# Kernel tuning notes

Measured on AMD Instinct MI355X. Metric: run time of the kernel, lower is better.

## Reference

```python
import jax, jax.numpy as jnp
import numpy as np

B = 1024      # Monte-Carlo samples (batch)
NX, NY = 8, 8 # lattice size
I = 3         # local Hilbert dim (hole, down, up)
H = 256       # hidden_dim
N_TARGET = 48 # target particle number
SZ = 0        # target magnetization sector


def setup_inputs() -> dict:
    key = jax.random.key(0)
    ks = jax.random.split(key, 8)
    f = jnp.float32
    samples = jax.random.randint(ks[0], (B, NX, NY), 0, 3)
    s_in = 1.0 / np.sqrt(2 * H)
    W1 = jax.random.normal(ks[1], (2 * I, 2 * H, H), f) * s_in
    W2 = jax.random.normal(ks[2], (2 * I, 2 * H, H), f) * s_in
    Wmerge = jax.random.normal(ks[3], (2 * H, H), f) * s_in
    b1 = jnp.full((H,), 0.01, f)
    b2 = jnp.full((H,), 0.01, f)
    s_l = 1.0 / np.sqrt(H)
    Wl1 = jax.random.normal(ks[4], (H, I), f) * s_l
    bl1 = jnp.zeros((I,), f)
    Wl2 = jax.random.normal(ks[5], (H, I), f) * s_l
    bl2 = jnp.zeros((I,), f)
    return {"samples": samples, "W1": W1, "b1": b1, "W2": W2, "b2": b2,
            "Wmerge": Wmerge, "Wl1": Wl1, "bl1": bl1, "Wl2": Wl2, "bl2": bl2}


def _gru_cell(sx, sy, hx, hy, W1, b1, W2, b2, Wmerge):
    # sx,sy: [B,I] one-hot neighbor inputs; hx,hy: [B,H] neighbor hiddens
    st = jnp.concatenate([hx, hy], axis=1)   # [B, 2H]
    inp = jnp.concatenate([sx, sy], axis=1)  # [B, 2I]
    # torch: einsum('ijk,lj->ikl', W, st) then einsum('li,ikl->lk', inp, .)
    pre1 = jnp.einsum('li,ijk,lj->lk', inp, W1, st)
    h_tilde = jnp.tanh(pre1 + b1)
    pre2 = jnp.einsum('li,ijk,lj->lk', inp, W2, st)
    u = jax.nn.sigmoid(pre2 + b2)
    return u * h_tilde + (1.0 - u) * (st @ Wmerge)


def _forward(samples, W1, b1, W2, b2, Wmerge, Wl1, bl1, Wl2, bl2):
    f = W1.dtype
    oh = jax.nn.one_hot(samples, I, dtype=f)  # [B,NX,NY,I]
    z_h = jnp.zeros((B, H), f)
    z_s = jnp.zeros((B, I), f)
    hid = {}
    bl_up = (N_TARGET + 2 * SZ) // 2
    bl_dn = (N_TARGET - 2 * SZ) // 2
    bl_hole = NX * NY - N_TARGET
    n_up = jnp.zeros((B,), f)
    n_dn = jnp.zeros((B,), f)
    log_a = jnp.zeros((B,), f)
    log_p = jnp.zeros((B,), f)
    k = 0  # number of already-sampled sites (static per step)
    for ny in range(NY):
        # snake (zig-zag) ordering over the 2D lattice
        xs = range(NX) if ny % 2 == 0 else range(NX - 1, -1, -1)
        dx = -1 if ny % 2 == 0 else 1
        for nx in xs:
            nxn = nx + dx
            sx = oh[:, nxn, ny] if 0 <= nxn < NX else z_s
            hx = hid.get((nxn, ny), z_h)
            sy = oh[:, nx, ny - 1] if ny > 0 else z_s
            hy = hid.get((nx, ny - 1), z_h)
            h = _gru_cell(sx, sy, hx, hy, W1, b1, W2, b2, Wmerge)
            hid[(nx, ny)] = h
            probs = jax.nn.softmax(h @ Wl1 + bl1, axis=1)          # [B,I]
            phase = jnp.pi * jax.nn.soft_sign(h @ Wl2 + bl2)       # [B,I]
            # enforce particle-number / magnetization sectors (heaviside masks)
            m_up = (bl_up - n_up > 0).astype(f)
            m_dn = (bl_dn - n_dn > 0).astype(f)
            m_hole = (bl_hole - (k - n_up - n_dn) > 0).astype(f)
            mask = jnp.stack([m_hole, m_dn, m_up], axis=1)         # [B,I]
            amp = probs * mask
            amp = amp / jnp.maximum(amp.sum(axis=1, keepdims=True), 1e-30)
            s = samples[:, nx, ny]
            sel = jax.nn.one_hot(s, I, dtype=f)
            log_a = log_a + jnp.log(jnp.clip((amp * sel).sum(axis=1), 1e-12))
            log_p = log_p + (phase * sel).sum(axis=1)
            n_up = n_up + (s == 2).astype(f)
            n_dn = n_dn + (s == 1).astype(f)
            k += 1
    return 0.5 * log_a, log_p


def reference(samples, W1, b1, W2, b2, Wmerge, Wl1, bl1, Wl2, bl2):
    return _forward(samples, W1, b1, W2, b2, Wmerge, Wl1, bl1, Wl2, bl2)
```

## Files before the change

kernel.cpp:

```cpp
#include <hip/hip_runtime.h>
#include <math.h>

#define Bsz 1024
#define Hd  256
#define MAXTILE 40
#define PERM_PER_CELL (MAXTILE*32)
#define WCSTRIDE (512*768)
#define GHALF (Bsz*768)
#define NPART 4

__global__ __launch_bounds__(256)
void build_wc(const float* __restrict__ W1, const float* __restrict__ W2,
              const float* __restrict__ Wm, float* __restrict__ Wc)
{
    size_t idx = (size_t)blockIdx.x * 256 + threadIdx.x;
    int col = (int)(idx % 768);
    size_t rem = idx / 768;
    int j = (int)(rem % 512);
    int c = (int)(rem / 512);
    int a = c >> 2, b = c & 3;
    float v;
    if (col < 256) {
        v = ((a < 3) ? W1[(size_t)a * 512 * 256 + j * 256 + col] : 0.f)
          + ((b < 3) ? W1[(size_t)(3 + b) * 512 * 256 + j * 256 + col] : 0.f);
    } else if (col < 512) {
        int cc = col - 256;
        v = ((a < 3) ? W2[(size_t)a * 512 * 256 + j * 256 + cc] : 0.f)
          + ((b < 3) ? W2[(size_t)(3 + b) * 512 * 256 + j * 256 + cc] : 0.f);
    } else {
        v = Wm[(size_t)j * 256 + (col - 512)];
    }
    Wc[idx] = v;
}

__global__ __launch_bounds__(256)
void bucketize(const int* __restrict__ samples, int* __restrict__ perm,
               int* __restrict__ tiletab)
{
    const int cell = blockIdx.x;
    const int t = threadIdx.x;
    const int ny = cell >> 3, ixs = cell & 7;
    const int nx  = (ny & 1) ? (7 - ixs) : ixs;
    const int dx  = (ny & 1) ? 1 : -1;
    const int nxn = nx + dx;
    const bool hasX = (nxn >= 0) && (nxn < 8);
    const bool hasY = (ny > 0);
    const int sx_off = nxn * 8 + ny;
    const int sy_off = nx * 8 + ny - 1;

    __shared__ int hist[16], cursor[16];
    int* pcell = perm + (size_t)cell * PERM_PER_CELL;
    for (int i = t; i < PERM_PER_CELL; i += 256) pcell[i] = -1;
    if (t < 16) hist[t] = 0;
    __syncthreads();

    int myc[4];
#pragma unroll
    for (int q = 0; q < 4; q++) {
        int l = t * 4 + q;
        int a = hasX ? samples[l * 64 + sx_off] : 3;
        int b = hasY ? samples[l * 64 + sy_off] : 3;
        myc[q] = a * 4 + b;
        atomicAdd(&hist[myc[q]], 1);
    }
    __syncthreads();

    if (t == 0) {
        int tile = 0, row = 0;
        for (int c = 0; c < 16; c++) {
            cursor[c] = row;
            int nt = (hist[c] + 31) >> 5;
            for (int k = 0; k < nt; k++) tiletab[cell * MAXTILE + tile + k] = c;
            tile += nt;
            row  += nt * 32;
        }
        for (; tile < MAXTILE; tile++) tiletab[cell * MAXTILE + tile] = -1;
    }
    __syncthreads();

#pragma unroll
    for (int q = 0; q < 4; q++) {
        int l = t * 4 + q;
        int pos = atomicAdd(&cursor[myc[q]], 1);
        pcell[pos] = l;
    }
}

#define BM 32
#define BN 64
#define BKt 32

__global__ __launch_bounds__(128)
void gemm_cell(const float* __restrict__ hx, const float* __restrict__ hy,
               const float* __restrict__ Wc, const int* __restrict__ perm,
               const int* __restrict__ tiletab, float* __restrict__ Gp,
               int cell, int kbeg, int kend)
{
    const int combo = tiletab[cell * MAXTILE + blockIdx.y];
    if (combo < 0) return;
    const int chunk = blockIdx.z;
    const int kbase = chunk << 7;
    const int hoff  = (chunk < 2) ? 0 : 256;
    int lo = (kbeg > kbase) ? kbeg : kbase;
    int hi = kbase + 128; if (kend < hi) hi = kend;
    const float* hsrc = (chunk < 2) ? hx : hy;
    const int k0 = blockIdx.x * BN;
    const float* Wsrc = Wc + (size_t)combo * WCSTRIDE;
    const int* pr = perm + (size_t)cell * PERM_PER_CELL + blockIdx.y * BM;
    float* Gout = Gp + (size_t)chunk * GHALF;

    const int t  = threadIdx.x;
    const int ar = t >> 2;
    const int aj = (t & 3) * 8;
    const int bj = t >> 4;
    const int bc = (t & 15) * 4;
    const int ty = t >> 4;
    const int tx = t & 15;

    __shared__ float As[BKt][BM];
    __shared__ float Bs[BKt][BN];
    __shared__ int rowidx[BM];
    if (t < BM) rowidx[t] = pr[t];
    const int myrow = pr[ar];

    float acc[4][4];
#pragma unroll
    for (int i = 0; i < 4; i++)
#pragma unroll
        for (int j = 0; j < 4; j++) acc[i][j] = 0.0f;

    for (int kk = lo; kk < hi; kk += BKt) {
        float4 a0 = make_float4(0.f, 0.f, 0.f, 0.f), a1 = a0;
        if (myrow >= 0) {
            const float* ap = hsrc + (size_t)myrow * Hd + (kk - hoff) + aj;
            a0 = *reinterpret_cast<const float4*>(ap);
            a1 = *reinterpret_cast<const float4*>(ap + 4);
        }
        const float* bp = Wsrc + (size_t)(kk + bj) * 768 + k0 + bc;
        float4 b0 = *reinterpret_cast<const float4*>(bp);
        float4 b1 = *reinterpret_cast<const float4*>(bp +  8 * 768);
        float4 b2 = *reinterpret_cast<const float4*>(bp + 16 * 768);
        float4 b3 = *reinterpret_cast<const float4*>(bp + 24 * 768);

        __syncthreads();
        As[aj + 0][ar] = a0.x; As[aj + 1][ar] = a0.y;
        As[aj + 2][ar] = a0.z; As[aj + 3][ar] = a0.w;
        As[aj + 4][ar] = a1.x; As[aj + 5][ar] = a1.y;
        As[aj + 6][ar] = a1.z; As[aj + 7][ar] = a1.w;
        *reinterpret_cast<float4*>(&Bs[bj     ][bc]) = b0;
        *reinterpret_cast<float4*>(&Bs[bj +  8][bc]) = b1;
        *reinterpret_cast<float4*>(&Bs[bj + 16][bc]) = b2;
        *reinterpret_cast<float4*>(&Bs[bj + 24][bc]) = b3;
        __syncthreads();

#pragma unroll
        for (int j = 0; j < BKt; j++) {
            float4 a = *reinterpret_cast<const float4*>(&As[j][ty * 4]);
            float4 b = *reinterpret_cast<const float4*>(&Bs[j][tx * 4]);
            float aa[4] = {a.x, a.y, a.z, a.w};
            float bb[4] = {b.x, b.y, b.z, b.w};
#pragma unroll
            for (int i = 0; i < 4; i++)
#pragma unroll
                for (int jj = 0; jj < 4; jj++)
                    acc[i][jj] = fmaf(aa[i], bb[jj], acc[i][jj]);
        }
    }
    __syncthreads();

#pragma unroll
    for (int i = 0; i < 4; i++) {
        int r = rowidx[ty * 4 + i];
        if (r >= 0) {
            float* gp = Gout + (size_t)r * 768 + k0 + tx * 4;
            float4 o = {acc[i][0], acc[i][1], acc[i][2], acc[i][3]};
            *reinterpret_cast<float4*>(gp) = o;
        }
    }
}

__global__ __launch_bounds__(256)
void combine_logprob(const float* __restrict__ Gp, const int* __restrict__ samples,
                     const float* __restrict__ b1, const float* __restrict__ b2,
                     const float* __restrict__ Wl1, const float* __restrict__ bl1,
                     const float* __restrict__ Wl2, const float* __restrict__ bl2,
                     float* __restrict__ hout, float* __restrict__ acc,
                     float* __restrict__ out, int s_off, int kcell)
{
    const int l = blockIdx.x;
    const int k = threadIdx.x;
    const float* g0 = Gp + (size_t)l * 768;

    float pre1 = b1[k], pre2 = b2[k], mg = 0.f;
#pragma unroll
    for (int z = 0; z < NPART; z++) {
        const float* g = g0 + (size_t)z * GHALF;
        pre1 += g[k];
        pre2 += g[256 + k];
        mg   += g[512 + k];
    }
    float ht = tanhf(pre1);
    float u  = 1.0f / (1.0f + expf(-pre2));
    float h  = u * ht + (1.0f - u) * mg;
    hout[(size_t)l * Hd + k] = h;

    float v[6];
    v[0] = h * Wl1[k * 3 + 0];
    v[1] = h * Wl1[k * 3 + 1];
    v[2] = h * Wl1[k * 3 + 2];
    v[3] = h * Wl2[k * 3 + 0];
    v[4] = h * Wl2[k * 3 + 1];
    v[5] = h * Wl2[k * 3 + 2];
#pragma unroll
    for (int m = 1; m < 64; m <<= 1)
#pragma unroll
        for (int i = 0; i < 6; i++) v[i] += __shfl_xor(v[i], m);

    __shared__ float red[4][6];
    if ((k & 63) == 0) {
#pragma unroll
        for (int i = 0; i < 6; i++) red[k >> 6][i] = v[i];
    }
    __syncthreads();

    if (k == 0) {
        float p1[3], p2[3];
#pragma unroll
        for (int i = 0; i < 3; i++) {
            p1[i] = red[0][i]     + red[1][i]     + red[2][i]     + red[3][i];
            p2[i] = red[0][3 + i] + red[1][3 + i] + red[2][3 + i] + red[3][3 + i];
        }
        float la, lp, nu, nd;
        if (kcell == 0) { la = 0.f; lp = 0.f; nu = 0.f; nd = 0.f; }
        else {
            la = acc[l];           lp = acc[Bsz + l];
            nu = acc[2 * Bsz + l]; nd = acc[3 * Bsz + l];
        }
        float z0 = p1[0] + bl1[0], z1 = p1[1] + bl1[1], z2 = p1[2] + bl1[2];
        float zm = fmaxf(z0, fmaxf(z1, z2));
        float e0 = expf(z0 - zm), e1 = expf(z1 - zm), e2 = expf(z2 - zm);
        float es = e0 + e1 + e2;
        float mh = (16.0f - ((float)kcell - nu - nd) > 0.0f) ? 1.0f : 0.0f;
        float md = (24.0f - nd > 0.0f) ? 1.0f : 0.0f;
        float mu = (24.0f - nu > 0.0f) ? 1.0f : 0.0f;
        float a0 = (e0 / es) * mh, a1 = (e1 / es) * md, a2 = (e2 / es) * mu;
        float asum = fmaxf(a0 + a1 + a2, 1e-30f);
        int sv = samples[l * 64 + s_off];
        float av = ((sv == 0) ? a0 : (sv == 1) ? a1 : a2) / asum;
        float q  = p2[sv] + bl2[sv];
        float ph = 3.14159265358979323846f * (q / (1.0f + fabsf(q)));
        la += logf(fmaxf(av, 1e-12f));
        lp += ph;
        nu += (sv == 2) ? 1.0f : 0.0f;
        nd += (sv == 1) ? 1.0f : 0.0f;
        acc[l] = la; acc[Bsz + l] = lp;
        acc[2 * Bsz + l] = nu; acc[3 * Bsz + l] = nd;
        if (kcell == 63) {
            out[l]       = 0.5f * la;
            out[Bsz + l] = lp;
        }
    }
}

extern "C" void kernel_launch(void* const* d_in, const int* in_sizes, int n_in,
                              void* d_out, int out_size, void* d_ws, size_t ws_size,
                              hipStream_t stream)
{
    const int*   samples = (const int*)  d_in[0];
    const float* W1  = (const float*)d_in[1];
    const float* b1  = (const float*)d_in[2];
    const float* W2  = (const float*)d_in[3];
    const float* b2  = (const float*)d_in[4];
    const float* Wm  = (const float*)d_in[5];
    const float* Wl1 = (const float*)d_in[6];
    const float* bl1 = (const float*)d_in[7];
    const float* Wl2 = (const float*)d_in[8];
    const float* bl2 = (const float*)d_in[9];

    float* ws   = (float*)d_ws;
    float* Hcol = ws;
    float* Gp   = Hcol + (size_t)8 * Bsz * Hd;
    float* acc  = Gp   + (size_t)NPART * GHALF;
    float* Wc   = acc  + 4 * Bsz;
    int*   perm    = (int*)(Wc + (size_t)16 * WCSTRIDE);
    int*   tiletab = perm + (size_t)64 * PERM_PER_CELL;
    float* out  = (float*)d_out;

    build_wc<<<dim3(16 * 512 * 768 / 256), dim3(256), 0, stream>>>(W1, W2, Wm, Wc);
    bucketize<<<dim3(64), dim3(256), 0, stream>>>(samples, perm, tiletab);

    int kcell = 0;
    for (int ny = 0; ny < 8; ny++) {
        const int x0  = (ny % 2 == 0) ? 0 : 7;
        const int dxs = (ny % 2 == 0) ? 1 : -1;
        const int dx  = (ny % 2 == 0) ? -1 : 1;
        for (int ix = 0; ix < 8; ix++) {
            const int nx  = x0 + ix * dxs;
            const int nxn = nx + dx;
            const bool hasX = (nxn >= 0 && nxn < 8);
            const bool hasY = (ny > 0);
            const float* hx = hasX ? (Hcol + (size_t)nxn * Bsz * Hd) : nullptr;
            const float* hy = hasY ? (Hcol + (size_t)nx  * Bsz * Hd) : nullptr;
            const int kbeg = hasX ? 0   : 256;
            const int kend = hasY ? 512 : 256;

            gemm_cell<<<dim3(12, MAXTILE, NPART), dim3(128), 0, stream>>>(
                hx, hy, Wc, perm, tiletab, Gp, kcell, kbeg, kend);

            combine_logprob<<<dim3(Bsz), dim3(256), 0, stream>>>(
                Gp, samples, b1, b2, Wl1, bl1, Wl2, bl2,
                Hcol + (size_t)nx * Bsz * Hd, acc, out, nx * 8 + ny, kcell);
            kcell++;
        }
    }
}
```

Baseline: 1.693 ms.

## Use split-bf16 MFMA GEMM with transposed weights for per-cell GRU products

Replaces the scalar FP32 tiled GEMM with a bf16 MFMA kernel. It emulates FP32 accuracy by splitting weights and hidden states into high and low bf16 parts and using three MFMAs per step. Weights are pre-transposed into K-contiguous bf16 layout and staged into XOR-swizzled shared memory. Hidden states are now stored as bf16 hi/lo pairs. This trades a small precision loss and triple MFMA work for matrix-core throughput and half-size weight traffic.

```diff
diff --git a/kernel.cpp b/kernel.cpp
--- a/kernel.cpp
+++ b/kernel.cpp
@@ -1,36 +1,44 @@
 #include <hip/hip_runtime.h>
+#include <hip/hip_bf16.h>
 #include <math.h>
 
 #define Bsz 1024
 #define Hd  256
 #define MAXTILE 40
 #define PERM_PER_CELL (MAXTILE*32)
-#define WCSTRIDE (512*768)
+#define WTSTRIDE (768*512)
 #define GHALF (Bsz*768)
 #define NPART 4
 
+typedef short bf16x8 __attribute__((ext_vector_type(8)));
+typedef float f32x4  __attribute__((ext_vector_type(4)));
+
 __global__ __launch_bounds__(256)
 void build_wc(const float* __restrict__ W1, const float* __restrict__ W2,
-              const float* __restrict__ Wm, float* __restrict__ Wc)
+              const float* __restrict__ Wm,
+              __hip_bfloat16* __restrict__ Wht, __hip_bfloat16* __restrict__ Wlt)
 {
     size_t idx = (size_t)blockIdx.x * 256 + threadIdx.x;
-    int col = (int)(idx % 768);
-    size_t rem = idx / 768;
-    int j = (int)(rem % 512);
-    int c = (int)(rem / 512);
+    int k = (int)(idx & 511);
+    size_t rem = idx >> 9;
+    int col = (int)(rem % 768);
+    int c = (int)(rem / 768);
     int a = c >> 2, b = c & 3;
     float v;
     if (col < 256) {
-        v = ((a < 3) ? W1[(size_t)a * 512 * 256 + j * 256 + col] : 0.f)
-          + ((b < 3) ? W1[(size_t)(3 + b) * 512 * 256 + j * 256 + col] : 0.f);
+        v = ((a < 3) ? W1[(size_t)a * 512 * 256 + k * 256 + col] : 0.f)
+          + ((b < 3) ? W1[(size_t)(3 + b) * 512 * 256 + k * 256 + col] : 0.f);
     } else if (col < 512) {
         int cc = col - 256;
-        v = ((a < 3) ? W2[(size_t)a * 512 * 256 + j * 256 + cc] : 0.f)
-          + ((b < 3) ? W2[(size_t)(3 + b) * 512 * 256 + j * 256 + cc] : 0.f);
+        v = ((a < 3) ? W2[(size_t)a * 512 * 256 + k * 256 + cc] : 0.f)
+          + ((b < 3) ? W2[(size_t)(3 + b) * 512 * 256 + k * 256 + cc] : 0.f);
     } else {
-        v = Wm[(size_t)j * 256 + (col - 512)];
-    }
-    Wc[idx] = v;
+        v = Wm[(size_t)k * 256 + (col - 512)];
+    }
+    __hip_bfloat16 vh = __float2bfloat16(v);
+    __hip_bfloat16 vl = __float2bfloat16(v - __bfloat162float(vh));
+    Wht[idx] = vh;
+    Wlt[idx] = vl;
 }
 
 __global__ __launch_bounds__(256)
@@ -86,96 +94,84 @@
     }
 }
 
-#define BM 32
-#define BN 64
-#define BKt 32
-
-__global__ __launch_bounds__(128)
-void gemm_cell(const float* __restrict__ hx, const float* __restrict__ hy,
-               const float* __restrict__ Wc, const int* __restrict__ perm,
-               const int* __restrict__ tiletab, float* __restrict__ Gp,
-               int cell, int kbeg, int kend)
+__global__ __launch_bounds__(256)
+void gemm_mfma(const __hip_bfloat16* __restrict__ hxh, const __hip_bfloat16* __restrict__ hxl,
+               const __hip_bfloat16* __restrict__ hyh, const __hip_bfloat16* __restrict__ hyl,
+               const __hip_bfloat16* __restrict__ Wht, const __hip_bfloat16* __restrict__ Wlt,
+               const int* __restrict__ perm, const int* __restrict__ tiletab,
+               float* __restrict__ Gp, int cell, int kbeg, int kend)
 {
     const int combo = tiletab[cell * MAXTILE + blockIdx.y];
     if (combo < 0) return;
     const int chunk = blockIdx.z;
     const int kbase = chunk << 7;
-    const int hoff  = (chunk < 2) ? 0 : 256;
-    int lo = (kbeg > kbase) ? kbeg : kbase;
-    int hi = kbase + 128; if (kend < hi) hi = kend;
-    const float* hsrc = (chunk < 2) ? hx : hy;
-    const int k0 = blockIdx.x * BN;
-    const float* Wsrc = Wc + (size_t)combo * WCSTRIDE;
-    const int* pr = perm + (size_t)cell * PERM_PER_CELL + blockIdx.y * BM;
+    const int lo = (kbeg > kbase) ? kbeg : kbase;
+    const int hi = (kend < kbase + 128) ? kend : (kbase + 128);
+    const int k0 = blockIdx.x * 64;
+    const int* pr = perm + (size_t)cell * PERM_PER_CELL + blockIdx.y * 32;
     float* Gout = Gp + (size_t)chunk * GHALF;
 
     const int t  = threadIdx.x;
-    const int ar = t >> 2;
-    const int aj = (t & 3) * 8;
-    const int bj = t >> 4;
-    const int bc = (t & 15) * 4;
-    const int ty = t >> 4;
-    const int tx = t & 15;
-
-    __shared__ float As[BKt][BM];
-    __shared__ float Bs[BKt][BN];
-    __shared__ int rowidx[BM];
-    if (t < BM) rowidx[t] = pr[t];
-    const int myrow = pr[ar];
-
-    float acc[4][4];
-#pragma unroll
-    for (int i = 0; i < 4; i++)
-#pragma unroll
-        for (int j = 0; j < 4; j++) acc[i][j] = 0.0f;
-
-    for (int kk = lo; kk < hi; kk += BKt) {
-        float4 a0 = make_float4(0.f, 0.f, 0.f, 0.f), a1 = a0;
-        if (myrow >= 0) {
-            const float* ap = hsrc + (size_t)myrow * Hd + (kk - hoff) + aj;
-            a0 = *reinterpret_cast<const float4*>(ap);
-            a1 = *reinterpret_cast<const float4*>(ap + 4);
-        }
-        const float* bp = Wsrc + (size_t)(kk + bj) * 768 + k0 + bc;
-        float4 b0 = *reinterpret_cast<const float4*>(bp);
-        float4 b1 = *reinterpret_cast<const float4*>(bp +  8 * 768);
-        float4 b2 = *reinterpret_cast<const float4*>(bp + 16 * 768);
-        float4 b3 = *reinterpret_cast<const float4*>(bp + 24 * 768);
-
+    const int w  = t >> 6;
+    const int l  = t & 63;
+    const int lr = l & 15;
+    const int lg = l >> 4;
+
+    __shared__ __align__(16) short Bh[64 * 128];
+    __shared__ __align__(16) short Bl[64 * 128];
+
+    f32x4 acc0 = {0.f, 0.f, 0.f, 0.f};
+    f32x4 acc1 = {0.f, 0.f, 0.f, 0.f};
+
+    if (lo < hi) {
+        const __hip_bfloat16* baseH = Wht + (size_t)combo * WTSTRIDE + kbase;
+        const __hip_bfloat16* baseL = Wlt + (size_t)combo * WTSTRIDE + kbase;
+        for (int i = t; i < 1024; i += 256) {
+            int c  = i >> 4;
+            int kq = i & 15;
+            int q  = c * 16 + (kq ^ (c & 7));
+            ((uint4*)Bh)[q] = *(const uint4*)(baseH + (size_t)(k0 + c) * 512 + kq * 8);
+            ((uint4*)Bl)[q] = *(const uint4*)(baseL + (size_t)(k0 + c) * 512 + kq * 8);
+        }
         __syncthreads();
-        As[aj + 0][ar] = a0.x; As[aj + 1][ar] = a0.y;
-        As[aj + 2][ar] = a0.z; As[aj + 3][ar] = a0.w;
-        As[aj + 4][ar] = a1.x; As[aj + 5][ar] = a1.y;
-        As[aj + 6][ar] = a1.z; As[aj + 7][ar] = a1.w;
-        *reinterpret_cast<float4*>(&Bs[bj     ][bc]) = b0;
-        *reinterpret_cast<float4*>(&Bs[bj +  8][bc]) = b1;
-        *reinterpret_cast<float4*>(&Bs[bj + 16][bc]) = b2;
-        *reinterpret_cast<float4*>(&Bs[bj + 24][bc]) = b3;
-        __syncthreads();
-
-#pragma unroll
-        for (int j = 0; j < BKt; j++) {
-            float4 a = *reinterpret_cast<const float4*>(&As[j][ty * 4]);
-            float4 b = *reinterpret_cast<const float4*>(&Bs[j][tx * 4]);
-            float aa[4] = {a.x, a.y, a.z, a.w};
-            float bb[4] = {b.x, b.y, b.z, b.w};
-#pragma unroll
-            for (int i = 0; i < 4; i++)
-#pragma unroll
-                for (int jj = 0; jj < 4; jj++)
-                    acc[i][jj] = fmaf(aa[i], bb[jj], acc[i][jj]);
-        }
-    }
-    __syncthreads();
-
-#pragma unroll
-    for (int i = 0; i < 4; i++) {
-        int r = rowidx[ty * 4 + i];
-        if (r >= 0) {
-            float* gp = Gout + (size_t)r * 768 + k0 + tx * 4;
-            float4 o = {acc[i][0], acc[i][1], acc[i][2], acc[i][3]};
-            *reinterpret_cast<float4*>(gp) = o;
-        }
+
+        const __hip_bfloat16* Hh = (chunk < 2) ? hxh : hyh;
+        const __hip_bfloat16* Hl = (chunk < 2) ? hxl : hyl;
+        const int hbase = kbase - ((chunk < 2) ? 0 : 256);
+        const int r0 = pr[lr];
+        const int r1 = pr[16 + lr];
+        const int cB = w * 16 + lr;
+
+#pragma unroll
+        for (int ks = 0; ks < 4; ks++) {
+            const int koff = hbase + ks * 32 + lg * 8;
+            bf16x8 a0h = (r0 >= 0) ? *(const bf16x8*)(Hh + (size_t)r0 * Hd + koff) : (bf16x8)0;
+            bf16x8 a0l = (r0 >= 0) ? *(const bf16x8*)(Hl + (size_t)r0 * Hd + koff) : (bf16x8)0;
+            bf16x8 a1h = (r1 >= 0) ? *(const bf16x8*)(Hh + (size_t)r1 * Hd + koff) : (bf16x8)0;
+            bf16x8 a1l = (r1 >= 0) ? *(const bf16x8*)(Hl + (size_t)r1 * Hd + koff) : (bf16x8)0;
+
+            const int kq = ks * 4 + lg;
+            const int q  = cB * 16 + (kq ^ (cB & 7));
+            bf16x8 bh = ((const bf16x8*)Bh)[q];
+            bf16x8 bl = ((const bf16x8*)Bl)[q];
+
+            acc0 = __builtin_amdgcn_mfma_f32_16x16x32_bf16(a0h, bh, acc0, 0, 0, 0);
+            acc0 = __builtin_amdgcn_mfma_f32_16x16x32_bf16(a0h, bl, acc0, 0, 0, 0);
+            acc0 = __builtin_amdgcn_mfma_f32_16x16x32_bf16(a0l, bh, acc0, 0, 0, 0);
+            acc1 = __builtin_amdgcn_mfma_f32_16x16x32_bf16(a1h, bh, acc1, 0, 0, 0);
+            acc1 = __builtin_amdgcn_mfma_f32_16x16x32_bf16(a1h, bl, acc1, 0, 0, 0);
+            acc1 = __builtin_amdgcn_mfma_f32_16x16x32_bf16(a1l, bh, acc1, 0, 0, 0);
+        }
+    }
+
+    const int colA = k0 + w * 16 + lr;
+#pragma unroll
+    for (int reg = 0; reg < 4; reg++) {
+        const int rl = 4 * lg + reg;
+        int ra = pr[rl];
+        if (ra >= 0) Gout[(size_t)ra * 768 + colA] = acc0[reg];
+        int rb = pr[16 + rl];
+        if (rb >= 0) Gout[(size_t)rb * 768 + colA] = acc1[reg];
     }
 }
 
@@ -184,8 +180,9 @@
                      const float* __restrict__ b1, const float* __restrict__ b2,
                      const float* __restrict__ Wl1, const float* __restrict__ bl1,
                      const float* __restrict__ Wl2, const float* __restrict__ bl2,
-                     float* __restrict__ hout, float* __restrict__ acc,
-                     float* __restrict__ out, int s_off, int kcell)
+                     __hip_bfloat16* __restrict__ houth, __hip_bfloat16* __restrict__ houtl,
+                     float* __restrict__ acc, float* __restrict__ out,
+                     int s_off, int kcell)
 {
     const int l = blockIdx.x;
     const int k = threadIdx.x;
@@ -202,7 +199,10 @@
     float ht = tanhf(pre1);
     float u  = 1.0f / (1.0f + expf(-pre2));
     float h  = u * ht + (1.0f - u) * mg;
-    hout[(size_t)l * Hd + k] = h;
+    __hip_bfloat16 hh = __float2bfloat16(h);
+    __hip_bfloat16 hl = __float2bfloat16(h - __bfloat162float(hh));
+    houth[(size_t)l * Hd + k] = hh;
+    houtl[(size_t)l * Hd + k] = hl;
 
     float v[6];
     v[0] = h * Wl1[k * 3 + 0];
@@ -277,16 +277,18 @@
     const float* Wl2 = (const float*)d_in[8];
     const float* bl2 = (const float*)d_in[9];
 
-    float* ws   = (float*)d_ws;
-    float* Hcol = ws;
-    float* Gp   = Hcol + (size_t)8 * Bsz * Hd;
-    float* acc  = Gp   + (size_t)NPART * GHALF;
-    float* Wc   = acc  + 4 * Bsz;
-    int*   perm    = (int*)(Wc + (size_t)16 * WCSTRIDE);
-    int*   tiletab = perm + (size_t)64 * PERM_PER_CELL;
-    float* out  = (float*)d_out;
-
-    build_wc<<<dim3(16 * 512 * 768 / 256), dim3(256), 0, stream>>>(W1, W2, Wm, Wc);
+    float* ws = (float*)d_ws;
+    float* Gp  = ws;
+    float* acc = Gp + (size_t)NPART * GHALF;
+    __hip_bfloat16* Hh  = (__hip_bfloat16*)(acc + 4 * Bsz);
+    __hip_bfloat16* Hl  = Hh + (size_t)8 * Bsz * Hd;
+    __hip_bfloat16* Wht = Hl + (size_t)8 * Bsz * Hd;
+    __hip_bfloat16* Wlt = Wht + (size_t)16 * WTSTRIDE;
+    int* perm    = (int*)(Wlt + (size_t)16 * WTSTRIDE);
+    int* tiletab = perm + (size_t)64 * PERM_PER_CELL;
+    float* out = (float*)d_out;
+
+    build_wc<<<dim3(16 * 768 * 512 / 256), dim3(256), 0, stream>>>(W1, W2, Wm, Wht, Wlt);
     bucketize<<<dim3(64), dim3(256), 0, stream>>>(samples, perm, tiletab);
 
     int kcell = 0;
@@ -299,17 +301,20 @@
             const int nxn = nx + dx;
             const bool hasX = (nxn >= 0 && nxn < 8);
             const bool hasY = (ny > 0);
-            const float* hx = hasX ? (Hcol + (size_t)nxn * Bsz * Hd) : nullptr;
-            const float* hy = hasY ? (Hcol + (size_t)nx  * Bsz * Hd) : nullptr;
+            const __hip_bfloat16* hxh = hasX ? (Hh + (size_t)nxn * Bsz * Hd) : nullptr;
+            const __hip_bfloat16* hxl = hasX ? (Hl + (size_t)nxn * Bsz * Hd) : nullptr;
+            const __hip_bfloat16* hyh = hasY ? (Hh + (size_t)nx  * Bsz * Hd) : nullptr;
+            const __hip_bfloat16* hyl = hasY ? (Hl + (size_t)nx  * Bsz * Hd) : nullptr;
             const int kbeg = hasX ? 0   : 256;
             const int kend = hasY ? 512 : 256;
 
-            gemm_cell<<<dim3(12, MAXTILE, NPART), dim3(128), 0, stream>>>(
-                hx, hy, Wc, perm, tiletab, Gp, kcell, kbeg, kend);
+            gemm_mfma<<<dim3(12, MAXTILE, NPART), dim3(256), 0, stream>>>(
+                hxh, hxl, hyh, hyl, Wht, Wlt, perm, tiletab, Gp, kcell, kbeg, kend);
 
             combine_logprob<<<dim3(Bsz), dim3(256), 0, stream>>>(
                 Gp, samples, b1, b2, Wl1, bl1, Wl2, bl2,
-                Hcol + (size_t)nx * Bsz * Hd, acc, out, nx * 8 + ny, kcell);
+                Hh + (size_t)nx * Bsz * Hd, Hl + (size_t)nx * Bsz * Hd,
+                acc, out, nx * 8 + ny, kcell);
             kcell++;
         }
     }
```

Result: slower. 1.958 ms (+15.7%).
